# Performance work log

Measured on AMD Instinct MI355X. Metric: run time of the kernel, lower is better.

## Reference

```python
import jax, jax.numpy as jnp
import numpy as np

IMG = 128          # img_wh
K = 10             # points_per_pixel
RADIUS = 0.005     # rasterization radius in NDC units
BIG = 1e10         # sentinel depth for pixels a point does not cover


def setup_inputs() -> dict:
    key = jax.random.key(0)
    k1, k2 = jax.random.split(key)
    B, P = 2, 2048
    # points near origin; camera at t=(0,0,2) looking down +z -> z_cam ~ 2
    points = jax.random.normal(k1, (B, P, 3), jnp.float32) * 0.4
    features = jax.random.uniform(k2, (B, P, 3), jnp.float32)  # RGB per point
    cam_R = jnp.broadcast_to(jnp.eye(3, dtype=jnp.float32), (B, 3, 3))
    cam_t = jnp.broadcast_to(jnp.array([0.0, 0.0, 2.0], jnp.float32), (B, 3))
    f = jnp.array(128.0, jnp.float32)  # focal length in pixels (in_ndc=False)
    return {"points": points, "features": features, "cam_R": cam_R,
            "cam_t": cam_t, "f": f}


def _render(points, features, cam_R, cam_t, f):
    B, P, _ = points.shape
    # PyTorch3D extrinsics: x_cam = x_world @ R + T (row vectors)
    cam = jnp.einsum('bpi,bij->bpj', points, cam_R) + cam_t[:, None, :]
    x, y, z = cam[..., 0], cam[..., 1], cam[..., 2]
    cx = cy = IMG / 2.0
    # perspective projection to pixel coords (screen-space camera).
    # NDC axis flips used by PyTorch3D cancel inside the squared distance,
    # so distances (the only thing rasterization uses) are convention-free.
    px = f * x / z + cx  # [B,P]
    py = f * y / z + cy
    pix = jnp.arange(IMG, dtype=jnp.float32) + 0.5  # pixel centers
    gy, gx = jnp.meshgrid(pix, pix, indexing='ij')  # [H,W]
    gx = gx.reshape(-1)  # [HW]
    gy = gy.reshape(-1)
    scale = 2.0 / IMG  # pixels -> NDC units (square image)
    dx = (px[:, None, :] - gx[None, :, None]) * scale  # [B,HW,P]
    dy = (py[:, None, :] - gy[None, :, None]) * scale
    dist2 = dx * dx + dy * dy                           # [B,HW,P]
    hit = (dist2 < RADIUS * RADIUS) & (z[:, None, :] > 1e-3)
    zm = jnp.where(hit, z[:, None, :], BIG)             # masked depth
    # z-buffer: K nearest covering points per pixel (ascending depth)
    neg_top, idx = jax.lax.top_k(-zm, K)                # [B,HW,K]
    zbuf = -neg_top
    valid = zbuf < BIG * 0.5
    d2k = jnp.take_along_axis(dist2, idx, axis=-1)      # [B,HW,K]
    # PointsRenderer weights: 1 - dist2/r^2, clamped to [0,1]
    alpha = jnp.where(valid, jnp.clip(1.0 - d2k / (RADIUS * RADIUS), 0.0, 1.0), 0.0)
    b_idx = jnp.arange(B)[:, None, None]
    featk = features[b_idx, idx]                        # [B,HW,K,C]
    # front-to-back alpha compositing: w_k = a_k * prod_{j<k}(1-a_j)
    one_m = 1.0 - alpha
    T = jnp.concatenate([jnp.ones_like(alpha[..., :1]),
                         jnp.cumprod(one_m, axis=-1)[..., :-1]], axis=-1)
    w = alpha * T
    images = jnp.einsum('bnk,bnkc->bnc', w, featk).reshape(B, IMG, IMG, -1)
    # depth image = nearest z, background = -1 (PyTorch3D convention)
    depth = jnp.where(valid[..., 0], zbuf[..., 0], -1.0).reshape(B, IMG, IMG)
    return images, depth


def reference(points, features, cam_R, cam_t, f):
    return _render(points, features, cam_R, cam_t, f)
```

## Files before the change

kernel.cpp:

```cpp
#include <hip/hip_runtime.h>


constexpr int   IMGC  = 128;
constexpr int   HWC   = IMGC * IMGC;
constexpr int   KTOP  = 10;
constexpr int   TILE  = 16;
constexpr int   TPB   = 256;
constexpr int   CAPT  = 768;
constexpr float BIGF  = 1e10f;
constexpr float R2C   = 2.5e-05f;
constexpr float SCALE = 0.015625f;

__launch_bounds__(TPB)
__global__ void render_kernel(const float* __restrict__ points,
                              const float* __restrict__ feats,
                              const float* __restrict__ camR,
                              const float* __restrict__ camT,
                              const float* __restrict__ fptr,
                              float* __restrict__ out,
                              int B, int P)
{
    __shared__ float4 cand[CAPT];
    __shared__ int    cnt;

    const int tilesPerB = (IMGC / TILE) * (IMGC / TILE);
    const int b    = blockIdx.x / tilesPerB;
    const int tile = blockIdx.x - b * tilesPerB;
    const int r0   = (tile >> 3) * TILE;
    const int c0   = (tile & 7) * TILE;

    if (threadIdx.x == 0) cnt = 0;
    __syncthreads();

    const float* R = camR + 9 * b;
    const float* t = camT + 3 * b;
    const float  f = fptr[0];
    const float R00=R[0],R01=R[1],R02=R[2],
                R10=R[3],R11=R[4],R12=R[5],
                R20=R[6],R21=R[7],R22=R[8];
    const float t0=t[0], t1=t[1], t2=t[2];

    for (int p = threadIdx.x; p < P; p += TPB) {
        const float* pp = points + ((size_t)b * P + p) * 3;
        float p0 = pp[0], p1 = pp[1], p2 = pp[2];
        float x = p0*R00 + p1*R10 + p2*R20 + t0;
        float y = p0*R01 + p1*R11 + p2*R21 + t1;
        float z = p0*R02 + p1*R12 + p2*R22 + t2;
        float px = __fadd_rn(__fdiv_rn(__fmul_rn(f, x), z), 64.0f);
        float py = __fadd_rn(__fdiv_rn(__fmul_rn(f, y), z), 64.0f);
        float fx = floorf(px), fy = floorf(py);
        if (!(fx >= (float)c0 && fx < (float)(c0 + TILE) &&
              fy >= (float)r0 && fy < (float)(r0 + TILE))) continue;
        float gx = fx + 0.5f, gy = fy + 0.5f;
        float dx = __fmul_rn(__fsub_rn(px, gx), SCALE);
        float dy = __fmul_rn(__fsub_rn(py, gy), SCALE);
        float d2 = __fadd_rn(__fmul_rn(dx, dx), __fmul_rn(dy, dy));
        if (d2 < R2C && z > 1e-3f) {
            int s = atomicAdd(&cnt, 1);
            if (s < CAPT) cand[s] = make_float4(px, py, z, __int_as_float(p));
        }
    }
    __syncthreads();
    const int n = cnt < CAPT ? cnt : CAPT;

    const int   col = c0 + (threadIdx.x & 15);
    const int   row = r0 + (threadIdx.x >> 4);
    const float gx  = col + 0.5f, gy = row + 0.5f;

    float zk[KTOP], d2k[KTOP];
    int   ik[KTOP];
#pragma unroll
    for (int j = 0; j < KTOP; ++j) { zk[j] = BIGF; d2k[j] = 0.0f; ik[j] = 0x7fffffff; }

    for (int j = 0; j < n; ++j) {
        float4 v = cand[j];
        if ((int)floorf(v.x) != col || (int)floorf(v.y) != row) continue;
        int pidx = __float_as_int(v.w);
        if (v.z < zk[KTOP-1] || (v.z == zk[KTOP-1] && pidx < ik[KTOP-1])) {
            float dx = __fmul_rn(__fsub_rn(v.x, gx), SCALE);
            float dy = __fmul_rn(__fsub_rn(v.y, gy), SCALE);
            float d2 = __fadd_rn(__fmul_rn(dx, dx), __fmul_rn(dy, dy));
            zk[KTOP-1] = v.z; d2k[KTOP-1] = d2; ik[KTOP-1] = pidx;
#pragma unroll
            for (int q = KTOP-1; q > 0; --q) {
                bool sw = (zk[q] < zk[q-1]) ||
                          (zk[q] == zk[q-1] && ik[q] < ik[q-1]);
                if (sw) {
                    float tz = zk[q];  zk[q]  = zk[q-1];  zk[q-1]  = tz;
                    float td = d2k[q]; d2k[q] = d2k[q-1]; d2k[q-1] = td;
                    int   ti = ik[q];  ik[q]  = ik[q-1];  ik[q-1]  = ti;
                }
            }
        }
    }

    float T = 1.0f, ccr = 0.0f, ccg = 0.0f, ccb = 0.0f;
#pragma unroll
    for (int j = 0; j < KTOP; ++j) {
        if (zk[j] < 0.5f * BIGF) {
            float a = 1.0f - d2k[j] / R2C;
            a = fminf(fmaxf(a, 0.0f), 1.0f);
            float w = a * T;
            const float* ft = feats + ((size_t)b * P + ik[j]) * 3;
            ccr += w * ft[0]; ccg += w * ft[1]; ccb += w * ft[2];
            T *= (1.0f - a);
        }
    }

    const int pix = row * IMGC + col;
    float* img = out + (size_t)(b * HWC + pix) * 3;
    img[0] = ccr; img[1] = ccg; img[2] = ccb;
    out[(size_t)B * HWC * 3 + (size_t)b * HWC + pix] =
        (zk[0] < 0.5f * BIGF) ? zk[0] : -1.0f;
}

extern "C" void kernel_launch(void* const* d_in, const int* in_sizes, int n_in,
                              void* d_out, int out_size, void* d_ws, size_t ws_size,
                              hipStream_t stream) {
    const float* points = (const float*)d_in[0];
    const float* feats  = (const float*)d_in[1];
    const float* camR   = (const float*)d_in[2];
    const float* camT   = (const float*)d_in[3];
    const float* fptr   = (const float*)d_in[4];

    const int B = in_sizes[3] / 3;
    const int P = in_sizes[0] / (3 * B);

    const int tilesPerB = (IMGC / TILE) * (IMGC / TILE);
    render_kernel<<<B * tilesPerB, TPB, 0, stream>>>(
        points, feats, camR, camT, fptr, (float*)d_out, B, P);
}
```

Baseline: 81.39 us.

## Switch to 8-row band blocks with per-row candidate buckets

Replaces the 16x16 tile decomposition with 8-row full-width bands per block. Candidates are bucketed per row in shared memory with a precomputed d2 and column. Each thread then handles 4 pixels, scanning only its row's bucket, which cuts the per-pixel scan length. The cost is fewer blocks (32 instead of 128), so each block does more serial work and GPU occupancy drops. The per-row cap of 96 could also overflow if points cluster in one row.

```diff
diff --git a/kernel.cpp b/kernel.cpp
--- a/kernel.cpp
+++ b/kernel.cpp
@@ -4,32 +4,30 @@
 constexpr int   IMGC  = 128;
 constexpr int   HWC   = IMGC * IMGC;
 constexpr int   KTOP  = 10;
-constexpr int   TILE  = 16;
+constexpr int   ROWS  = 8;
+constexpr int   CAPR  = 96;
 constexpr int   TPB   = 256;
-constexpr int   CAPT  = 768;
 constexpr float BIGF  = 1e10f;
 constexpr float R2C   = 2.5e-05f;
 constexpr float SCALE = 0.015625f;
 
 __launch_bounds__(TPB)
-__global__ void render_kernel(const float* __restrict__ points,
-                              const float* __restrict__ feats,
-                              const float* __restrict__ camR,
-                              const float* __restrict__ camT,
-                              const float* __restrict__ fptr,
-                              float* __restrict__ out,
-                              int B, int P)
+__global__ void render_band_kernel(const float* __restrict__ points,
+                                   const float* __restrict__ feats,
+                                   const float* __restrict__ camR,
+                                   const float* __restrict__ camT,
+                                   const float* __restrict__ fptr,
+                                   float* __restrict__ out,
+                                   int B, int P)
 {
-    __shared__ float4 cand[CAPT];
-    __shared__ int    cnt;
+    __shared__ float4 bucket[ROWS][CAPR];
+    __shared__ int    cntRow[ROWS];
 
-    const int tilesPerB = (IMGC / TILE) * (IMGC / TILE);
-    const int b    = blockIdx.x / tilesPerB;
-    const int tile = blockIdx.x - b * tilesPerB;
-    const int r0   = (tile >> 3) * TILE;
-    const int c0   = (tile & 7) * TILE;
+    const int b    = blockIdx.x >> 4;
+    const int band = blockIdx.x & 15;
+    const int r0   = band * ROWS;
 
-    if (threadIdx.x == 0) cnt = 0;
+    if (threadIdx.x < ROWS) cntRow[threadIdx.x] = 0;
     __syncthreads();
 
     const float* R = camR + 9 * b;
@@ -49,69 +47,74 @@
         float px = __fadd_rn(__fdiv_rn(__fmul_rn(f, x), z), 64.0f);
         float py = __fadd_rn(__fdiv_rn(__fmul_rn(f, y), z), 64.0f);
         float fx = floorf(px), fy = floorf(py);
-        if (!(fx >= (float)c0 && fx < (float)(c0 + TILE) &&
-              fy >= (float)r0 && fy < (float)(r0 + TILE))) continue;
+        if (!(fx >= 0.0f && fx <= 127.0f &&
+              fy >= (float)r0 && fy < (float)(r0 + ROWS))) continue;
+        int col = (int)fx;
         float gx = fx + 0.5f, gy = fy + 0.5f;
         float dx = __fmul_rn(__fsub_rn(px, gx), SCALE);
         float dy = __fmul_rn(__fsub_rn(py, gy), SCALE);
         float d2 = __fadd_rn(__fmul_rn(dx, dx), __fmul_rn(dy, dy));
         if (d2 < R2C && z > 1e-3f) {
-            int s = atomicAdd(&cnt, 1);
-            if (s < CAPT) cand[s] = make_float4(px, py, z, __int_as_float(p));
+            int r = (int)fy - r0;
+            int s = atomicAdd(&cntRow[r], 1);
+            if (s < CAPR)
+                bucket[r][s] = make_float4(z, d2, __int_as_float(p),
+                                           __int_as_float(col));
         }
     }
     __syncthreads();
-    const int n = cnt < CAPT ? cnt : CAPT;
 
-    const int   col = c0 + (threadIdx.x & 15);
-    const int   row = r0 + (threadIdx.x >> 4);
-    const float gx  = col + 0.5f, gy = row + 0.5f;
+    const int lrow = threadIdx.x >> 5;
+    const int row  = r0 + lrow;
+    const int cbase = (threadIdx.x & 31) * 4;
+    int cnt = cntRow[lrow];
+    if (cnt > CAPR) cnt = CAPR;
 
-    float zk[KTOP], d2k[KTOP];
-    int   ik[KTOP];
+    for (int c = cbase; c < cbase + 4; ++c) {
+        float zk[KTOP], d2k[KTOP];
+        int   ik[KTOP];
 #pragma unroll
-    for (int j = 0; j < KTOP; ++j) { zk[j] = BIGF; d2k[j] = 0.0f; ik[j] = 0x7fffffff; }
+        for (int j = 0; j < KTOP; ++j) { zk[j] = BIGF; d2k[j] = 0.0f; ik[j] = 0x7fffffff; }
 
-    for (int j = 0; j < n; ++j) {
-        float4 v = cand[j];
-        if ((int)floorf(v.x) != col || (int)floorf(v.y) != row) continue;
-        int pidx = __float_as_int(v.w);
-        if (v.z < zk[KTOP-1] || (v.z == zk[KTOP-1] && pidx < ik[KTOP-1])) {
-            float dx = __fmul_rn(__fsub_rn(v.x, gx), SCALE);
-            float dy = __fmul_rn(__fsub_rn(v.y, gy), SCALE);
-            float d2 = __fadd_rn(__fmul_rn(dx, dx), __fmul_rn(dy, dy));
-            zk[KTOP-1] = v.z; d2k[KTOP-1] = d2; ik[KTOP-1] = pidx;
+        for (int j = 0; j < cnt; ++j) {
+            float4 v = bucket[lrow][j];
+            if (__float_as_int(v.w) != c) continue;
+            float vz = v.x;
+            int   pi = __float_as_int(v.z);
+            if (vz < zk[KTOP-1] || (vz == zk[KTOP-1] && pi < ik[KTOP-1])) {
+                zk[KTOP-1] = vz; d2k[KTOP-1] = v.y; ik[KTOP-1] = pi;
 #pragma unroll
-            for (int q = KTOP-1; q > 0; --q) {
-                bool sw = (zk[q] < zk[q-1]) ||
-                          (zk[q] == zk[q-1] && ik[q] < ik[q-1]);
-                if (sw) {
-                    float tz = zk[q];  zk[q]  = zk[q-1];  zk[q-1]  = tz;
-                    float td = d2k[q]; d2k[q] = d2k[q-1]; d2k[q-1] = td;
-                    int   ti = ik[q];  ik[q]  = ik[q-1];  ik[q-1]  = ti;
+                for (int q = KTOP-1; q > 0; --q) {
+                    bool sw = (zk[q] < zk[q-1]) ||
+                              (zk[q] == zk[q-1] && ik[q] < ik[q-1]);
+                    if (sw) {
+                        float tz = zk[q];  zk[q]  = zk[q-1];  zk[q-1]  = tz;
+                        float td = d2k[q]; d2k[q] = d2k[q-1]; d2k[q-1] = td;
+                        int   ti = ik[q];  ik[q]  = ik[q-1];  ik[q-1]  = ti;
+                    }
                 }
             }
         }
+
+        float T = 1.0f, c0f = 0.0f, c1f = 0.0f, c2f = 0.0f;
+#pragma unroll
+        for (int j = 0; j < KTOP; ++j) {
+            if (zk[j] < 0.5f * BIGF) {
+                float a = 1.0f - d2k[j] / R2C;
+                a = fminf(fmaxf(a, 0.0f), 1.0f);
+                float w = a * T;
+                const float* ft = feats + ((size_t)b * P + ik[j]) * 3;
+                c0f += w * ft[0]; c1f += w * ft[1]; c2f += w * ft[2];
+                T *= (1.0f - a);
+            }
+        }
+
+        const int pix = row * IMGC + c;
+        float* img = out + (size_t)(b * HWC + pix) * 3;
+        img[0] = c0f; img[1] = c1f; img[2] = c2f;
+        out[(size_t)B * HWC * 3 + (size_t)b * HWC + pix] =
+            (zk[0] < 0.5f * BIGF) ? zk[0] : -1.0f;
     }
-
-    float T = 1.0f, ccr = 0.0f, ccg = 0.0f, ccb = 0.0f;
-#pragma unroll
-    for (int j = 0; j < KTOP; ++j) {
-        if (zk[j] < 0.5f * BIGF) {
-            float a = 1.0f - d2k[j] / R2C;
-            a = fminf(fmaxf(a, 0.0f), 1.0f);
-            float w = a * T;
-            const float* ft = feats + ((size_t)b * P + ik[j]) * 3;
-            ccr += w * ft[0]; ccg += w * ft[1]; ccb += w * ft[2];
-            T *= (1.0f - a);
-        }
-    }
-
-    const int pix = row * IMGC + col;
-    float* img = out + (size_t)(b * HWC + pix) * 3;
-    img[0] = ccr; img[1] = ccg; img[2] = ccb;
-    out[(size_t)B * HWC * 3 + (size_t)b * HWC + pix] =
-        (zk[0] < 0.5f * BIGF) ? zk[0] : -1.0f;
 }
 
 extern "C" void kernel_launch(void* const* d_in, const int* in_sizes, int n_in,
@@ -126,7 +129,6 @@
     const int B = in_sizes[3] / 3;
     const int P = in_sizes[0] / (3 * B);
 
-    const int tilesPerB = (IMGC / TILE) * (IMGC / TILE);
-    render_kernel<<<B * tilesPerB, TPB, 0, stream>>>(
+    render_band_kernel<<<B * 16, TPB, 0, stream>>>(
         points, feats, camR, camT, fptr, (float*)d_out, B, P);
 }
```

Measured after the change: 98.15 us. +20.6%, slower.

## Switch from 16x16 tiles to one block per image row with precomputed buckets

Applied to the files above, without the earlier changes.

Each block now handles one image row (B*128 blocks) rather than a 16x16 tile (B*64 blocks). Every block still projects all points but keeps only those landing in its row. Candidates are stored with precomputed depth, squared distance, point index and column, so the per-pixel scan compares one integer and skips recomputing distances. The top-K insertion is written as explicit scalar compare-swaps to keep the lists in registers. In exchange, the projection work is duplicated across twice as many blocks, half the threads sit idle in the per-pixel phase, and the per-row candidate cap drops to 128.

```diff
diff --git a/kernel.cpp b/kernel.cpp
--- a/kernel.cpp
+++ b/kernel.cpp
@@ -3,31 +3,44 @@
 
 constexpr int   IMGC  = 128;
 constexpr int   HWC   = IMGC * IMGC;
-constexpr int   KTOP  = 10;
-constexpr int   TILE  = 16;
+constexpr int   CAPR  = 128;
 constexpr int   TPB   = 256;
-constexpr int   CAPT  = 768;
 constexpr float BIGF  = 1e10f;
 constexpr float R2C   = 2.5e-05f;
 constexpr float SCALE = 0.015625f;
 
+#define CSWAP(za, da, ia, zb, db, ib)                                  \
+    {                                                                  \
+        bool sw_ = (zb < za) || (zb == za && ib < ia);                 \
+        float tz_ = za, td_ = da; int ti_ = ia;                        \
+        if (sw_) { za = zb; da = db; ia = ib;                          \
+                   zb = tz_; db = td_; ib = ti_; }                     \
+    }
+
+#define COMPOSE(zq, dq, iq)                                            \
+    if (zq < 0.5f * BIGF) {                                            \
+        float a_ = 1.0f - dq / R2C;                                    \
+        a_ = fminf(fmaxf(a_, 0.0f), 1.0f);                             \
+        float w_ = a_ * T;                                             \
+        const float* ft_ = feats + ((size_t)b * P + iq) * 3;           \
+        cr += w_ * ft_[0]; cg += w_ * ft_[1]; cb += w_ * ft_[2];       \
+        T *= (1.0f - a_);                                              \
+    }
+
 __launch_bounds__(TPB)
-__global__ void render_kernel(const float* __restrict__ points,
-                              const float* __restrict__ feats,
-                              const float* __restrict__ camR,
-                              const float* __restrict__ camT,
-                              const float* __restrict__ fptr,
-                              float* __restrict__ out,
-                              int B, int P)
+__global__ void render_row_kernel(const float* __restrict__ points,
+                                  const float* __restrict__ feats,
+                                  const float* __restrict__ camR,
+                                  const float* __restrict__ camT,
+                                  const float* __restrict__ fptr,
+                                  float* __restrict__ out,
+                                  int B, int P)
 {
-    __shared__ float4 cand[CAPT];
+    __shared__ float4 bucket[CAPR];
     __shared__ int    cnt;
 
-    const int tilesPerB = (IMGC / TILE) * (IMGC / TILE);
-    const int b    = blockIdx.x / tilesPerB;
-    const int tile = blockIdx.x - b * tilesPerB;
-    const int r0   = (tile >> 3) * TILE;
-    const int c0   = (tile & 7) * TILE;
+    const int b   = blockIdx.x >> 7;
+    const int row = blockIdx.x & 127;
 
     if (threadIdx.x == 0) cnt = 0;
     __syncthreads();
@@ -39,6 +52,7 @@
                 R10=R[3],R11=R[4],R12=R[5],
                 R20=R[6],R21=R[7],R22=R[8];
     const float t0=t[0], t1=t[1], t2=t[2];
+    const float rowF = (float)row;
 
     for (int p = threadIdx.x; p < P; p += TPB) {
         const float* pp = points + ((size_t)b * P + p) * 3;
@@ -49,69 +63,68 @@
         float px = __fadd_rn(__fdiv_rn(__fmul_rn(f, x), z), 64.0f);
         float py = __fadd_rn(__fdiv_rn(__fmul_rn(f, y), z), 64.0f);
         float fx = floorf(px), fy = floorf(py);
-        if (!(fx >= (float)c0 && fx < (float)(c0 + TILE) &&
-              fy >= (float)r0 && fy < (float)(r0 + TILE))) continue;
+        if (!(fx >= 0.0f && fx <= 127.0f && fy == rowF)) continue;
         float gx = fx + 0.5f, gy = fy + 0.5f;
         float dx = __fmul_rn(__fsub_rn(px, gx), SCALE);
         float dy = __fmul_rn(__fsub_rn(py, gy), SCALE);
         float d2 = __fadd_rn(__fmul_rn(dx, dx), __fmul_rn(dy, dy));
         if (d2 < R2C && z > 1e-3f) {
             int s = atomicAdd(&cnt, 1);
-            if (s < CAPT) cand[s] = make_float4(px, py, z, __int_as_float(p));
+            if (s < CAPR)
+                bucket[s] = make_float4(z, d2, __int_as_float(p),
+                                        __int_as_float((int)fx));
         }
     }
     __syncthreads();
-    const int n = cnt < CAPT ? cnt : CAPT;
+    int n = cnt; if (n > CAPR) n = CAPR;
 
-    const int   col = c0 + (threadIdx.x & 15);
-    const int   row = r0 + (threadIdx.x >> 4);
-    const float gx  = col + 0.5f, gy = row + 0.5f;
+    if (threadIdx.x < IMGC) {
+        const int col = threadIdx.x;
 
-    float zk[KTOP], d2k[KTOP];
-    int   ik[KTOP];
-#pragma unroll
-    for (int j = 0; j < KTOP; ++j) { zk[j] = BIGF; d2k[j] = 0.0f; ik[j] = 0x7fffffff; }
+        float z0=BIGF,z1=BIGF,z2=BIGF,z3=BIGF,z4=BIGF,
+              z5=BIGF,z6=BIGF,z7=BIGF,z8=BIGF,z9=BIGF;
+        float d0=0,d1=0,d2_=0,d3=0,d4=0,d5=0,d6=0,d7=0,d8=0,d9=0;
+        int   i0=0x7fffffff,i1=0x7fffffff,i2=0x7fffffff,i3=0x7fffffff,
+              i4=0x7fffffff,i5=0x7fffffff,i6=0x7fffffff,i7=0x7fffffff,
+              i8=0x7fffffff,i9=0x7fffffff;
 
-    for (int j = 0; j < n; ++j) {
-        float4 v = cand[j];
-        if ((int)floorf(v.x) != col || (int)floorf(v.y) != row) continue;
-        int pidx = __float_as_int(v.w);
-        if (v.z < zk[KTOP-1] || (v.z == zk[KTOP-1] && pidx < ik[KTOP-1])) {
-            float dx = __fmul_rn(__fsub_rn(v.x, gx), SCALE);
-            float dy = __fmul_rn(__fsub_rn(v.y, gy), SCALE);
-            float d2 = __fadd_rn(__fmul_rn(dx, dx), __fmul_rn(dy, dy));
-            zk[KTOP-1] = v.z; d2k[KTOP-1] = d2; ik[KTOP-1] = pidx;
-#pragma unroll
-            for (int q = KTOP-1; q > 0; --q) {
-                bool sw = (zk[q] < zk[q-1]) ||
-                          (zk[q] == zk[q-1] && ik[q] < ik[q-1]);
-                if (sw) {
-                    float tz = zk[q];  zk[q]  = zk[q-1];  zk[q-1]  = tz;
-                    float td = d2k[q]; d2k[q] = d2k[q-1]; d2k[q-1] = td;
-                    int   ti = ik[q];  ik[q]  = ik[q-1];  ik[q-1]  = ti;
-                }
+        for (int j = 0; j < n; ++j) {
+            float4 v = bucket[j];
+            if (__float_as_int(v.w) != col) continue;
+            float vz = v.x, vd = v.y;
+            int   vi = __float_as_int(v.z);
+            if (vz < z9 || (vz == z9 && vi < i9)) {
+                z9 = vz; d9 = vd; i9 = vi;
+                CSWAP(z8, d8, i8, z9, d9, i9);
+                CSWAP(z7, d7, i7, z8, d8, i8);
+                CSWAP(z6, d6, i6, z7, d7, i7);
+                CSWAP(z5, d5, i5, z6, d6, i6);
+                CSWAP(z4, d4, i4, z5, d5, i5);
+                CSWAP(z3, d3, i3, z4, d4, i4);
+                CSWAP(z2, d2_, i2, z3, d3, i3);
+                CSWAP(z1, d1, i1, z2, d2_, i2);
+                CSWAP(z0, d0, i0, z1, d1, i1);
             }
         }
+
+        float T = 1.0f, cr = 0.0f, cg = 0.0f, cb = 0.0f;
+        COMPOSE(z0, d0, i0)
+        COMPOSE(z1, d1, i1)
+        COMPOSE(z2, d2_, i2)
+        COMPOSE(z3, d3, i3)
+        COMPOSE(z4, d4, i4)
+        COMPOSE(z5, d5, i5)
+        COMPOSE(z6, d6, i6)
+        COMPOSE(z7, d7, i7)
+        COMPOSE(z8, d8, i8)
+        COMPOSE(z9, d9, i9)
+
+        const int pix = row * IMGC + col;
+        float* img = out + (size_t)(b * HWC + pix) * 3;
+        img[0] = cr; img[1] = cg; img[2] = cb;
+        out[(size_t)B * HWC * 3 + (size_t)b * HWC + pix] =
+            (z0 < 0.5f * BIGF) ? z0 : -1.0f;
     }
-
-    float T = 1.0f, ccr = 0.0f, ccg = 0.0f, ccb = 0.0f;
-#pragma unroll
-    for (int j = 0; j < KTOP; ++j) {
-        if (zk[j] < 0.5f * BIGF) {
-            float a = 1.0f - d2k[j] / R2C;
-            a = fminf(fmaxf(a, 0.0f), 1.0f);
-            float w = a * T;
-            const float* ft = feats + ((size_t)b * P + ik[j]) * 3;
-            ccr += w * ft[0]; ccg += w * ft[1]; ccb += w * ft[2];
-            T *= (1.0f - a);
-        }
-    }
-
-    const int pix = row * IMGC + col;
-    float* img = out + (size_t)(b * HWC + pix) * 3;
-    img[0] = ccr; img[1] = ccg; img[2] = ccb;
-    out[(size_t)B * HWC * 3 + (size_t)b * HWC + pix] =
-        (zk[0] < 0.5f * BIGF) ? zk[0] : -1.0f;
 }
 
 extern "C" void kernel_launch(void* const* d_in, const int* in_sizes, int n_in,
@@ -126,7 +139,6 @@
     const int B = in_sizes[3] / 3;
     const int P = in_sizes[0] / (3 * B);
 
-    const int tilesPerB = (IMGC / TILE) * (IMGC / TILE);
-    render_kernel<<<B * tilesPerB, TPB, 0, stream>>>(
+    render_row_kernel<<<B * IMGC, TPB, 0, stream>>>(
         points, feats, camR, camT, fptr, (float*)d_out, B, P);
 }
```

After: 72.40 us. 11.0% less time.
